# Optimization experiments

Measured on AMD Instinct MI355X. Metric: run time of the kernel, lower is better.

## Reference

```python
import jax, jax.numpy as jnp
import numpy as np

IN_CH = 128
HID = 64
EPS = 1e-5
N_NODES = 20000
E_UND = 80000


def _build_line_graph(edge_index, num_nodes):
    # dedupe to unique undirected edges (src<dst); line-graph nodes = these edges
    src = np.asarray(edge_index[0]); dst = np.asarray(edge_index[1])
    m = src < dst
    u, v = src[m], dst[m]
    key = u.astype(np.int64) * num_nodes + v.astype(np.int64)
    _, first = np.unique(key, return_index=True)
    u, v = u[first], v[first]
    E = u.shape[0]
    # incidence lists grouped by node; all ordered pairs of co-incident edges
    nodes = np.concatenate([u, v])
    eids = np.concatenate([np.arange(E), np.arange(E)])
    order = np.argsort(nodes, kind="stable")
    nodes_s, eids_s = nodes[order], eids[order]
    counts = np.bincount(nodes_s, minlength=num_nodes)
    offsets = np.concatenate([np.zeros(1, np.int64), np.cumsum(counts)])
    grp_start = offsets[nodes_s]
    reps = counts[nodes_s]
    total = int(reps.sum())
    starts = np.cumsum(reps) - reps
    idx = np.arange(total) - np.repeat(starts, reps) + np.repeat(grp_start, reps)
    row = np.repeat(eids_s, reps); col = eids_s[idx]
    keep = row != col
    return np.stack([u, v]), np.stack([row[keep], col[keep]])


def _gcn_conv(x, src, dst, W, b):
    # PyG GCNConv: add self loops, symmetric D^-1/2 (A+I) D^-1/2 normalization
    N = x.shape[0]
    sl = jnp.arange(N)
    s = jnp.concatenate([src, sl]); d = jnp.concatenate([dst, sl])
    deg = jax.ops.segment_sum(jnp.ones(s.shape[0], x.dtype), d, num_segments=N)
    dinv = jax.lax.rsqrt(jnp.maximum(deg, 1.0))
    h = x @ W
    msg = h[s] * (dinv[s] * dinv[d])[:, None]
    return jax.ops.segment_sum(msg, d, num_segments=N) + b


def _edge_scores(line_x, lsrc, ldst, W1, b1, gamma1, beta1, W2, b2):
    h = _gcn_conv(line_x, lsrc, ldst, W1, b1)
    mu = h.mean(0); var = h.var(0)  # BatchNorm1d, training-mode batch stats
    h = jax.nn.relu(gamma1 * (h - mu) * jax.lax.rsqrt(var + EPS) + beta1)
    return jax.nn.sigmoid(_gcn_conv(h, lsrc, ldst, W2, b2))[:, 0]


def _cluster(clean, topk_idx, num_nodes):
    ti = np.asarray(topk_idx)
    sel_src = np.asarray(clean[0])[ti]; sel_dst = np.asarray(clean[1])[ti]
    n2c = np.arange(num_nodes)
    rev = sel_dst[::-1]
    _, fi = np.unique(rev, return_index=True)
    last = sel_dst.shape[0] - 1 - fi
    n2c[sel_dst[last]] = sel_src[last]
    uniq = np.unique(n2c)
    M = int(uniq.shape[0])
    old_to_new = np.full(num_nodes, -1, np.int64)
    old_to_new[uniq] = np.arange(M)
    return old_to_new[n2c], uniq, M


def _make_graph():
    rng = np.random.default_rng(0)
    a = rng.integers(0, N_NODES, E_UND)
    off = rng.integers(1, N_NODES, E_UND)
    b = (a + off) % N_NODES  # no self loops
    u = np.minimum(a, b); v = np.maximum(a, b)
    return np.stack([np.concatenate([u, v]), np.concatenate([v, u])]).astype(np.int64)


def _make_params():
    ks = jax.random.split(jax.random.key(0), 4)
    x = jax.random.normal(ks[0], (N_NODES, IN_CH), jnp.float32)
    W1 = jax.random.normal(ks[1], (IN_CH, HID), jnp.float32) / np.float32(np.sqrt(IN_CH))
    b1 = jnp.zeros((HID,), jnp.float32)
    gamma1 = jnp.ones((HID,), jnp.float32)
    beta1 = jnp.zeros((HID,), jnp.float32)
    W2 = jax.random.normal(ks[2], (HID, 1), jnp.float32) / np.float32(np.sqrt(HID))
    b2 = jnp.zeros((1,), jnp.float32)
    return x, W1, b1, gamma1, beta1, W2, b2


def setup_inputs() -> dict:
    x, W1, b1, gamma1, beta1, W2, b2 = _make_params()
    return {
        "x": x, "W1": W1, "b1": b1, "gamma1": gamma1, "beta1": beta1,
        "W2": W2, "b2": b2,
        "edge_index": jnp.asarray(_make_graph()),
        "batch": jnp.zeros((N_NODES,), jnp.int32),
    }


def reference(x, W1, b1, gamma1, beta1, W2, b2, edge_index, batch):
    N = x.shape[0]
    clean, line_ei = _build_line_graph(edge_index, N)
    csrc = jnp.asarray(clean[0]); cdst = jnp.asarray(clean[1])
    lsrc = jnp.asarray(line_ei[0]); ldst = jnp.asarray(line_ei[1])
    line_x = 0.5 * (x[csrc] + x[cdst])  # line-graph node features
    scores = _edge_scores(line_x, lsrc, ldst, W1, b1, gamma1, beta1, W2, b2)
    E_c = scores.shape[0]
    k = max(1, min(E_c // 2, N // 2))
    _, topk_idx = jax.lax.top_k(scores, k)
    new_indices, uniq, M = _cluster(clean, topk_idx, N)
    ni = jnp.asarray(new_indices)
    # aggregate: per-cluster mean of member node features (code's weights are unused)
    counts = jax.ops.segment_sum(jnp.ones(N, x.dtype), ni, num_segments=M)
    x_pool = jax.ops.segment_sum(x, ni, num_segments=M) / counts[:, None]
    batch_pool = batch[jnp.asarray(uniq)]
    # build_new_edges: relabel, drop self loops, coalesce (sorted unique)
    ei = np.asarray(edge_index)
    ns = new_indices[ei[0]]; nd = new_indices[ei[1]]
    keep = ns != nd
    pk = ns[keep] * M + nd[keep]
    upk = np.unique(pk)
    edge_index_pool = jnp.asarray(np.stack([upk // M, upk % M]))
    return (x_pool, edge_index_pool, batch_pool, scores, ni)
```

## Files before the change

kernel.cpp:

```cpp
#include <hip/hip_runtime.h>
#include <stdint.h>

typedef unsigned long long u64;
typedef unsigned int u32;

#define NND 20000
#define EUA 160000
#define EFE 80000
#define ICH 128
#define HIDC 64
#define SCAN_BS 256
#define NB_N ((NND + 255) / 256)
#define NB_EU ((EUA + 255) / 256)
#define NB_EF ((EFE + 255) / 256)
#define NB_E64 ((EFE * HIDC + 255) / 256)
#define NB_X ((NND * ICH + 255) / 256)
#define NSCAN_B ((NND + SCAN_BS - 1) / SCAN_BS)
#define HIST_BLOCKS 128
#define GEB 64
#define XS_PAD 132
#define NCHAIN 4096
#define OUT_MAX_INIT 3000000
#define BK64 64
#define SEL_BINS 4096


__global__ void kScanA(const int* __restrict__ in, int* __restrict__ out,
                       int* __restrict__ bsums, int n) {
    __shared__ int sh[SCAN_BS];
    int tid = threadIdx.x;
    int i = blockIdx.x * SCAN_BS + tid;
    int v = (i < n) ? in[i] : 0;
    sh[tid] = v;
    __syncthreads();
    for (int o = 1; o < SCAN_BS; o <<= 1) {
        int t = (tid >= o) ? sh[tid - o] : 0;
        __syncthreads();
        sh[tid] += t;
        __syncthreads();
    }
    if (i < n) out[i] = sh[tid] - v;
    if (tid == SCAN_BS - 1) bsums[blockIdx.x] = sh[tid];
}
__global__ void kScanB(int* __restrict__ out, const int* __restrict__ bsums,
                       int n, int nb, int* __restrict__ totalDst) {
    __shared__ int sh[160];
    int tid = threadIdx.x;
    if (tid <= nb) sh[tid] = (tid < nb) ? bsums[tid] : 0;
    __syncthreads();
    if (tid == 0) {
        int acc = 0;
        for (int i = 0; i < nb; i++) { int t = sh[i]; sh[i] = acc; acc += t; }
        sh[nb] = acc;
    }
    __syncthreads();
    int i = blockIdx.x * SCAN_BS + tid;
    if (i < n) out[i] += sh[blockIdx.x];
    if (i == 0) {
        int tot = sh[nb];
        out[n] = tot;
        *totalDst = tot;
    }
}

__global__ void kFilterScatter64(const int* __restrict__ ei, int* __restrict__ cnt,
                                 int* __restrict__ bucketV) {
    int i = blockIdx.x * 256 + threadIdx.x;
    if (i >= EUA) return;
    int s = ei[i], d = ei[EUA + i];
    if (s < d) {
        int p = atomicAdd(&cnt[s], 1);
        bucketV[(s << 6) + p] = d;
    }
}
__global__ void kRankSort64(const int* __restrict__ in, int* __restrict__ out,
                            const int* __restrict__ lenA, int* __restrict__ ucnt) {
    int a = blockIdx.x;
    int len = lenA[a];
    int base = a << 6;
    for (int j = threadIdx.x; j < len; j += 64) {
        int v = in[base + j];
        int r = 0;
        for (int i = 0; i < len; i++) {
            int w = in[base + i];
            r += (w < v) || (w == v && i < j);
        }
        out[base + r] = v;
    }
    __syncthreads();
    int c = 0;
    for (int j = threadIdx.x; j < len; j += 64)
        c += (j == 0) || (out[base + j] != out[base + j - 1]);
#pragma unroll
    for (int o = 32; o > 0; o >>= 1) c += __shfl_down(c, o, 64);
    if (threadIdx.x == 0) ucnt[a] = c;
}
__global__ void kCompactInc(const int* __restrict__ arr, const int* __restrict__ cnt,
                            const int* __restrict__ uoff, int* __restrict__ eU,
                            int* __restrict__ eV, int* __restrict__ icnt) {
    int u = blockIdx.x * 256 + threadIdx.x;
    if (u >= NND) return;
    int s = u << 6, e = s + cnt[u], o = uoff[u];
    int myc = 0;
    for (int i = s; i < e; i++)
        if (i == s || arr[i] != arr[i - 1]) {
            int v = arr[i];
            eU[o] = u; eV[o] = v; o++;
            atomicAdd(&icnt[v], 1);
            myc++;
        }
    if (myc) atomicAdd(&icnt[u], myc);
}

__global__ void kIncScatterDinv64(const int* __restrict__ eU, const int* __restrict__ eV,
                                  const int* __restrict__ scal, int* __restrict__ itmp,
                                  int* __restrict__ ilist, const int* __restrict__ icnt,
                                  float* __restrict__ dinv) {
    int e = blockIdx.x * 256 + threadIdx.x;
    if (e >= scal[0]) return;
    int u = eU[e], v = eV[e];
    ilist[(u << 6) + atomicAdd(&itmp[u], 1)] = e;
    ilist[(v << 6) + atomicAdd(&itmp[v], 1)] = e;
    dinv[e] = rsqrtf((float)(icnt[u] + icnt[v] - 1));
}

__global__ void kGemm(const float* __restrict__ x, const float* __restrict__ W1,
                      const int* __restrict__ eU, const int* __restrict__ eV,
                      const int* __restrict__ scal, float* __restrict__ h) {
    __shared__ float W1s[ICH][HIDC];
    __shared__ float xs[GEB][XS_PAD];
    int t = threadIdx.x;
    int E = scal[0];
    int e0 = blockIdx.x * GEB;
    if (e0 >= E) return;

    {
        const float4* Wv = (const float4*)W1;
        float4* Ws = (float4*)&W1s[0][0];
        for (int i = t; i < ICH * HIDC / 4; i += 256) Ws[i] = Wv[i];
    }
    {
        int eb = t >> 2, q = t & 3;
        int e = e0 + eb;
        if (e < E) {
            int u = eU[e], v = eV[e];
            const float4* xu = (const float4*)(x + (size_t)u * ICH) + q * 8;
            const float4* xv = (const float4*)(x + (size_t)v * ICH) + q * 8;
            float* xd = &xs[eb][q * 32];
#pragma unroll
            for (int i = 0; i < 8; i++) {
                float4 a = xu[i], b = xv[i];
                xd[i * 4 + 0] = 0.5f * (a.x + b.x);
                xd[i * 4 + 1] = 0.5f * (a.y + b.y);
                xd[i * 4 + 2] = 0.5f * (a.z + b.z);
                xd[i * 4 + 3] = 0.5f * (a.w + b.w);
            }
        }
    }
    __syncthreads();

    int cg4 = (t & 15) * 4;
    int es = t >> 4;
    float a00=0,a01=0,a02=0,a03=0, a10=0,a11=0,a12=0,a13=0;
    float a20=0,a21=0,a22=0,a23=0, a30=0,a31=0,a32=0,a33=0;
#pragma unroll 4
    for (int k = 0; k < ICH; k++) {
        float4 wv = *(const float4*)&W1s[k][cg4];
        float x0 = xs[es][k], x1 = xs[es + 16][k];
        float x2 = xs[es + 32][k], x3 = xs[es + 48][k];
        a00 += x0 * wv.x; a01 += x0 * wv.y; a02 += x0 * wv.z; a03 += x0 * wv.w;
        a10 += x1 * wv.x; a11 += x1 * wv.y; a12 += x1 * wv.z; a13 += x1 * wv.w;
        a20 += x2 * wv.x; a21 += x2 * wv.y; a22 += x2 * wv.z; a23 += x2 * wv.w;
        a30 += x3 * wv.x; a31 += x3 * wv.y; a32 += x3 * wv.z; a33 += x3 * wv.w;
    }
    int e;
    e = e0 + es;
    if (e < E) *(float4*)&h[(size_t)e * HIDC + cg4] = make_float4(a00, a01, a02, a03);
    e = e0 + es + 16;
    if (e < E) *(float4*)&h[(size_t)e * HIDC + cg4] = make_float4(a10, a11, a12, a13);
    e = e0 + es + 32;
    if (e < E) *(float4*)&h[(size_t)e * HIDC + cg4] = make_float4(a20, a21, a22, a23);
    e = e0 + es + 48;
    if (e < E) *(float4*)&h[(size_t)e * HIDC + cg4] = make_float4(a30, a31, a32, a33);
}

__global__ void kSGather(const float* __restrict__ h, const float* __restrict__ dinv,
                         const int* __restrict__ icnt, const int* __restrict__ ilist,
                         float* __restrict__ S) {
    int n = blockIdx.x;
    int c = threadIdx.x;
    int base = n << 6, len = icnt[n];
    float acc = 0.f;
    for (int j = 0; j < len; j++) {
        int ed = ilist[base + j];
        acc += h[(size_t)ed * HIDC + c] * dinv[ed];
    }
    S[(size_t)n * HIDC + c] = acc;
}
__global__ void kConv1Red1(const float* __restrict__ h, const float* __restrict__ S,
                           const float* __restrict__ dinv, const int* __restrict__ eU,
                           const int* __restrict__ eV, const float* __restrict__ b1,
                           const int* __restrict__ scal, float* __restrict__ h2,
                           float* __restrict__ partial) {
    int t = threadIdx.x;
    int g = blockIdx.x * 4 + (t >> 6);
    int c = t & 63;
    int E = scal[0];
    float bc = b1[c];
    float acc = 0.f;
    for (int e = g; e < E; e += NCHAIN) {
        float a = dinv[e];
        float v = a * (S[(size_t)eU[e] * HIDC + c] + S[(size_t)eV[e] * HIDC + c]) -
                  a * a * h[(size_t)e * HIDC + c] + bc;
        h2[(size_t)e * HIDC + c] = v;
        acc += v;
    }
    partial[g * HIDC + c] = acc;
}
__global__ void kRed1v(const float* __restrict__ h2, const int* __restrict__ scal,
                       const float* __restrict__ muvar, float* __restrict__ partial) {
    int t = threadIdx.x;
    int g = blockIdx.x * 4 + (t >> 6);
    int c = t & 63;
    int E = scal[0];
    float m = muvar[c];
    float acc = 0.f;
    for (int e = g; e < E; e += NCHAIN) {
        float d = h2[(size_t)e * HIDC + c] - m;
        acc += d * d;
    }
    partial[g * HIDC + c] = acc;
}
__global__ void kRed2(const float* __restrict__ partial, const int* __restrict__ scal,
                      float* __restrict__ muvar, int pass) {
    __shared__ float sh[4][HIDC];
    int t = threadIdx.x;
    int q = t >> 6, c = t & 63;
    float acc = 0.f;
    int g0 = q * (NCHAIN / 4);
    for (int g = g0; g < g0 + NCHAIN / 4; g++) acc += partial[g * HIDC + c];
    sh[q][c] = acc;
    __syncthreads();
    if (q == 0) {
        float s = ((sh[0][c] + sh[1][c]) + sh[2][c]) + sh[3][c];
        muvar[pass * HIDC + c] = s / (float)scal[0];
    }
}
__global__ void kNormZ(const float* __restrict__ h2, const float* __restrict__ muvar,
                       const float* __restrict__ gamma1, const float* __restrict__ beta1,
                       const float* __restrict__ W2, const int* __restrict__ scal,
                       float* __restrict__ z) {
    int idx = blockIdx.x * 256 + threadIdx.x;
    int e = idx >> 6;
    if (e >= scal[0]) return;
    int c = idx & 63;
    float t = gamma1[c] * (h2[idx] - muvar[c]) * rsqrtf(muvar[HIDC + c] + 1e-5f) + beta1[c];
    t = t > 0.f ? t : 0.f;
    float p = t * W2[c];
#pragma unroll
    for (int o = 32; o > 0; o >>= 1) p += __shfl_down(p, o, 64);
    if (c == 0) z[e] = p;
}
__global__ void kS2(const float* __restrict__ z, const float* __restrict__ dinv,
                    const int* __restrict__ icnt, const int* __restrict__ ilist,
                    float* __restrict__ S2) {
    int n = blockIdx.x * 256 + threadIdx.x;
    if (n >= NND) return;
    int base = n << 6, len = icnt[n];
    float acc = 0.f;
    for (int j = 0; j < len; j++) {
        int e = ilist[base + j];
        acc += z[e] * dinv[e];
    }
    S2[n] = acc;
}
__global__ void kScore(const float* __restrict__ z, const float* __restrict__ S2,
                       const float* __restrict__ dinv, const int* __restrict__ eU,
                       const int* __restrict__ eV, const float* __restrict__ b2,
                       const int* __restrict__ scal, float* __restrict__ score,
                       u64* __restrict__ okey, int* __restrict__ krem,
                       u64* __restrict__ pref, u64* __restrict__ minOkey) {
    int e = blockIdx.x * 256 + threadIdx.x;
    if (e < NND) minOkey[e] = ~0ULL;
    int E = scal[0];
    if (e >= E) return;
    if (e == 0) {
        int k = E / 2;
        if (k > NND / 2) k = NND / 2;
        if (k < 1) k = 1;
        *krem = k;
        *pref = 1ULL << 48;
    }
    float a = dinv[e];
    float l = a * (S2[eU[e]] + S2[eV[e]]) - a * a * z[e] + b2[0];
    float s = 1.f / (1.f + expf(-l));
    score[e] = s;
    u32 b = __float_as_uint(s);
    b = (b >> 31) ? ~b : (b | 0x80000000u);
    okey[e] = (((u64)b) << 17) | (u32)(0x1FFFFu - (u32)e);
}

__global__ void kHist(const u64* __restrict__ okey, const int* __restrict__ scal,
                      int* __restrict__ hist, const u64* __restrict__ pref,
                      u64 maskHi, int shift) {
    __shared__ int sh[4][SEL_BINS];
    int t = threadIdx.x;
    for (int j = t; j < 4 * SEL_BINS; j += 256) ((int*)sh)[j] = 0;
    __syncthreads();
    int wv = t >> 6;
    int E = scal[0];
    u64 p = *pref;
    for (int e = blockIdx.x * 256 + t; e < E; e += HIST_BLOCKS * 256) {
        u64 kk = okey[e];
        if ((kk & maskHi) == p)
            atomicAdd(&sh[wv][(int)((kk >> shift) & (SEL_BINS - 1))], 1);
    }
    __syncthreads();
    for (int j = t; j < SEL_BINS; j += 256) {
        int v = sh[0][j] + sh[1][j] + sh[2][j] + sh[3][j];
        if (v) atomicAdd(&hist[j], v);
    }
}
__global__ void kSelPass(int* __restrict__ hist, u64* __restrict__ pref,
                         int* __restrict__ krem, int shift) {
    __shared__ int sh[SEL_BINS];
    __shared__ int aux[256];
    __shared__ int shKr;
    int t = threadIdx.x;
    int g = 0;
#pragma unroll
    for (int j = 0; j < 16; j++) {
        int v = hist[16 * t + j];
        sh[16 * t + j] = v;
        hist[16 * t + j] = 0;
        g += v;
    }
    if (t == 0) shKr = *krem;
    aux[t] = g;
    __syncthreads();
    for (int o = 1; o < 256; o <<= 1) {
        int v = (t + o < 256) ? aux[t + o] : 0;
        __syncthreads();
        aux[t] += v;
        __syncthreads();
    }
    int kr = shKr;
    int suf = aux[t] - g;
    if (suf < kr && kr <= suf + g) {
        int cum = suf, found = 16 * t;
        for (int b = 16 * t + 15; b >= 16 * t; b--) {
            int hc = sh[b];
            if (cum + hc >= kr) { found = b; break; }
            cum += hc;
        }
        *krem = kr - cum;
        *pref |= ((u64)found) << shift;
    }
}

__global__ void kMinKeyInit(const u64* __restrict__ okey, const int* __restrict__ eV,
                            const int* __restrict__ scal, const u64* __restrict__ pref,
                            u64* __restrict__ minOkey, int* __restrict__ n2c) {
    int i = blockIdx.x * 256 + threadIdx.x;
    if (i < NND) n2c[i] = i;
    if (i < scal[0]) {
        u64 k = okey[i];
        if (k >= *pref) atomicMin(&minOkey[eV[i]], k);
    }
}
__global__ void kN2cSet(const u64* __restrict__ okey, const int* __restrict__ eU,
                        const int* __restrict__ eV, const int* __restrict__ scal,
                        const u64* __restrict__ pref, const u64* __restrict__ minOkey,
                        int* __restrict__ n2c) {
    int e = blockIdx.x * 256 + threadIdx.x;
    if (e >= scal[0]) return;
    u64 k = okey[e];
    int v = eV[e];
    if (k >= *pref && k == minOkey[v]) n2c[v] = eU[e];
}
__global__ void kPresent(const int* __restrict__ n2c, int* __restrict__ present) {
    int n = blockIdx.x * 256 + threadIdx.x;
    if (n < NND) present[n2c[n]] = 1;
}

__global__ void kNiXacc(const float* __restrict__ x, const int* __restrict__ n2c,
                        const int* __restrict__ o2n, int* __restrict__ ni,
                        int* __restrict__ ccnt, float* __restrict__ dout) {
    int idx = blockIdx.x * 256 + threadIdx.x;
    if (idx >= NND * ICH) return;
    int n = idx >> 7, c = idx & 127;
    int m = o2n[n2c[n]];
    atomicAdd(&dout[(size_t)m * ICH + c], x[idx]);
    if (c == 0) {
        ni[n] = m;
        atomicAdd(&ccnt[m], 1);
    }
}
__global__ void kXdivCEcount(float* __restrict__ dout, const int* __restrict__ ccnt,
                             const int* __restrict__ scal, const int* __restrict__ ei,
                             const int* __restrict__ ni, int* __restrict__ ecnt2) {
    int idx = blockIdx.x * 256 + threadIdx.x;
    if (idx < scal[2] * ICH) dout[idx] /= (float)ccnt[idx >> 7];
    if (idx < EUA) {
        int a = ni[ei[idx]], b = ni[ei[EUA + idx]];
        if (a != b) atomicAdd(&ecnt2[a], 1);
    }
}

__global__ void kCEscatter(const int* __restrict__ ei, const int* __restrict__ ni,
                           const int* __restrict__ eoff2, int* __restrict__ etmp2,
                           int* __restrict__ bkD) {
    int i = blockIdx.x * 256 + threadIdx.x;
    if (i >= EUA) return;
    int a = ni[ei[i]], b = ni[ei[EUA + i]];
    if (a != b) {
        int p = eoff2[a] + atomicAdd(&etmp2[a], 1);
        bkD[p] = b;
    }
}
__global__ void kRankSort(const int* __restrict__ in, int* __restrict__ out,
                          const int* __restrict__ offA, int* __restrict__ ucnt) {
    int a = blockIdx.x;
    int s = offA[a], e = offA[a + 1], len = e - s;
    for (int j = threadIdx.x; j < len; j += 64) {
        int v = in[s + j];
        int r = 0;
        for (int i = 0; i < len; i++) {
            int w = in[s + i];
            r += (w < v) || (w == v && i < j);
        }
        out[s + r] = v;
    }
    __syncthreads();
    int c = 0;
    for (int j = threadIdx.x; j < len; j += 64)
        c += (j == 0) || (out[s + j] != out[s + j - 1]);
#pragma unroll
    for (int o = 32; o > 0; o >>= 1) c += __shfl_down(c, o, 64);
    if (threadIdx.x == 0) ucnt[a] = c;
}
__global__ void kCEwriteTail(const int* __restrict__ bkD2, const int* __restrict__ eoff2,
                             const int* __restrict__ ueoff, const int* __restrict__ scal,
                             const int* __restrict__ batch, const int* __restrict__ present,
                             const int* __restrict__ o2n, const float* __restrict__ score,
                             const int* __restrict__ ni, float* __restrict__ dout) {
    int i = blockIdx.x * 256 + threadIdx.x;
    int E = scal[0], M = scal[2], Ep = scal[3];
    size_t base = (size_t)M * ICH;
    if (i < NND) {
        int s = eoff2[i], e = eoff2[i + 1];
        float* r0 = dout + base;
        float* r1 = r0 + Ep;
        int o = ueoff[i];
        for (int j = s; j < e; j++)
            if (j == s || bkD2[j] != bkD2[j - 1]) {
                r0[o] = (float)i;
                r1[o] = (float)bkD2[j];
                o++;
            }
    }
    size_t tb = base + 2 * (size_t)Ep;
    if (i < NND && present[i]) dout[tb + o2n[i]] = (float)batch[i];
    if (i < E) dout[tb + M + i] = score[i];
    if (i < NND) dout[tb + M + E + i] = (float)ni[i];
}

extern "C" void kernel_launch(void* const* d_in, const int* in_sizes, int n_in,
                              void* d_out, int out_size, void* d_ws, size_t ws_size,
                              hipStream_t stream) {
    (void)in_sizes; (void)n_in; (void)ws_size;
    const float* x = (const float*)d_in[0];
    const float* W1 = (const float*)d_in[1];
    const float* b1 = (const float*)d_in[2];
    const float* gamma1 = (const float*)d_in[3];
    const float* beta1 = (const float*)d_in[4];
    const float* W2 = (const float*)d_in[5];
    const float* b2 = (const float*)d_in[6];
    const int* ei = (const int*)d_in[7];
    const int* batch = (const int*)d_in[8];
    float* dout = (float*)d_out;

    char* w = (char*)d_ws;
    size_t off = 0;
    auto carve = [&](size_t bytes) -> void* {
        off = (off + 255) & ~(size_t)255;
        void* p = w + off;
        off += bytes;
        return p;
    };
    char* zero0 = w;
    int* cnt = (int*)carve(NND * 4);
    int* itmp = (int*)carve(NND * 4);
    int* icnt = (int*)carve(NND * 4);
    int* present = (int*)carve(NND * 4);
    int* ccnt = (int*)carve(NND * 4);
    int* ecnt2 = (int*)carve(NND * 4);
    int* etmp2 = (int*)carve(NND * 4);
    int* scal = (int*)carve(16 * 4);
    int* hist = (int*)carve(SEL_BINS * 4);
    size_t zeroBytes = off;
    int* ucnt = (int*)carve(NND * 4);
    int* uoff = (int*)carve((NND + 2) * 4);
    int* bsums = (int*)carve((NSCAN_B + 2) * 4);
    int* n2c = (int*)carve(NND * 4);
    int* o2n = (int*)carve((NND + 2) * 4);
    int* niArr = (int*)carve(NND * 4);
    int* eoff2 = (int*)carve((NND + 2) * 4);
    int* uecnt = (int*)carve(NND * 4);
    int* ueoff = (int*)carve((NND + 2) * 4);
    int* bucketV = (int*)carve((size_t)NND * BK64 * 4);
    int* bucketS = (int*)carve((size_t)NND * BK64 * 4);
    int* eU = (int*)carve(EFE * 4);
    int* eV = (int*)carve(EFE * 4);
    int* ilist = (int*)carve((size_t)NND * BK64 * 4);
    int* ilistS = (int*)carve((size_t)NND * BK64 * 4);
    int* bkD = (int*)carve(EUA * 4);
    int* bkD2 = (int*)carve(EUA * 4);
    u64* okey = (u64*)carve(EFE * 8);
    u64* minOkey = (u64*)carve(NND * 8);
    u64* dpref = (u64*)carve(8);
    float* dinv = (float*)carve(EFE * 4);
    float* h = (float*)carve((size_t)EFE * HIDC * 4);
    float* h2 = (float*)carve((size_t)EFE * HIDC * 4);
    float* Snode = (float*)carve((size_t)NND * HIDC * 4);
    float* partial = (float*)carve((size_t)NCHAIN * HIDC * 4);
    float* muvar = (float*)carve(128 * 4);
    float* zArr = (float*)carve(EFE * 4);
    float* S2 = (float*)carve(NND * 4);
    float* score = (float*)carve(EFE * 4);

    auto scan = [&](const int* in, int* outp, int* totalDst) {
        kScanA<<<NSCAN_B, SCAN_BS, 0, stream>>>(in, outp, bsums, NND);
        kScanB<<<NSCAN_B, SCAN_BS, 0, stream>>>(outp, bsums, NND, NSCAN_B, totalDst);
    };

    size_t outInit = (size_t)out_size;
    if (outInit > OUT_MAX_INIT) outInit = OUT_MAX_INIT;
    hipMemsetAsync(zero0, 0, zeroBytes, stream);
    hipMemsetAsync(d_out, 0, outInit * 4, stream);

    kFilterScatter64<<<NB_EU, 256, 0, stream>>>(ei, cnt, bucketV);
    kRankSort64<<<NND, 64, 0, stream>>>(bucketV, bucketS, cnt, ucnt);
    scan(ucnt, uoff, scal + 0);
    kCompactInc<<<NB_N, 256, 0, stream>>>(bucketS, cnt, uoff, eU, eV, icnt);

    kIncScatterDinv64<<<NB_EF, 256, 0, stream>>>(eU, eV, scal, itmp, ilist, icnt, dinv);
    kRankSort64<<<NND, 64, 0, stream>>>(ilist, ilistS, icnt, ucnt);

    kGemm<<<(EFE + GEB - 1) / GEB, 256, 0, stream>>>(x, W1, eU, eV, scal, h);
    kSGather<<<NND, HIDC, 0, stream>>>(h, dinv, icnt, ilistS, Snode);
    kConv1Red1<<<NCHAIN / 4, 256, 0, stream>>>(h, Snode, dinv, eU, eV, b1, scal, h2, partial);
    kRed2<<<1, 256, 0, stream>>>(partial, scal, muvar, 0);
    kRed1v<<<NCHAIN / 4, 256, 0, stream>>>(h2, scal, muvar, partial);
    kRed2<<<1, 256, 0, stream>>>(partial, scal, muvar, 1);
    kNormZ<<<NB_E64, 256, 0, stream>>>(h2, muvar, gamma1, beta1, W2, scal, zArr);

    kS2<<<NB_N, 256, 0, stream>>>(zArr, dinv, icnt, ilistS, S2);
    kScore<<<NB_EF, 256, 0, stream>>>(zArr, S2, dinv, eU, eV, b2, scal, score, okey,
                                      scal + 1, dpref, minOkey);

    for (int p = 0; p < 4; p++) {
        int shift = 36 - 12 * p;
        u64 maskHi = (~0ULL) << (shift + 12);
        kHist<<<HIST_BLOCKS, 256, 0, stream>>>(okey, scal, hist, dpref, maskHi, shift);
        kSelPass<<<1, 256, 0, stream>>>(hist, dpref, scal + 1, shift);
    }

    kMinKeyInit<<<NB_EF, 256, 0, stream>>>(okey, eV, scal, dpref, minOkey, n2c);
    kN2cSet<<<NB_EF, 256, 0, stream>>>(okey, eU, eV, scal, dpref, minOkey, n2c);
    kPresent<<<NB_N, 256, 0, stream>>>(n2c, present);
    scan(present, o2n, scal + 2);
    kNiXacc<<<NB_X, 256, 0, stream>>>(x, n2c, o2n, niArr, ccnt, dout);
    kXdivCEcount<<<NB_X, 256, 0, stream>>>(dout, ccnt, scal, ei, niArr, ecnt2);

    scan(ecnt2, eoff2, scal + 4);
    kCEscatter<<<NB_EU, 256, 0, stream>>>(ei, niArr, eoff2, etmp2, bkD);
    kRankSort<<<NND, 64, 0, stream>>>(bkD, bkD2, eoff2, uecnt);
    scan(uecnt, ueoff, scal + 3);
    kCEwriteTail<<<NB_EF, 256, 0, stream>>>(bkD2, eoff2, ueoff, scal, batch, present,
                                            o2n, score, niArr, dout);
}
```

Measured before the change: 401.4 us.

## Fuse radix-select passes by replaying prefix in each histogram block; merge cluster kernels

Removes the four single-block kSelPass launches by keeping one histogram per pass and having every kHistR block (and the min-key kernel) recompute the selected prefix from all earlier histograms. The three kernels for min-key init, n2c set and present marking become two, with the cluster id decoded straight from the winning key's edge index. This cuts kernel launches and serial single-block steps, but every block now redundantly repeats up to four block-wide scans over 4096-bin histograms.

```diff
diff --git a/kernel.cpp b/kernel.cpp
--- a/kernel.cpp
+++ b/kernel.cpp
@@ -278,19 +278,11 @@
                        const float* __restrict__ dinv, const int* __restrict__ eU,
                        const int* __restrict__ eV, const float* __restrict__ b2,
                        const int* __restrict__ scal, float* __restrict__ score,
-                       u64* __restrict__ okey, int* __restrict__ krem,
-                       u64* __restrict__ pref, u64* __restrict__ minOkey) {
+                       u64* __restrict__ okey, u64* __restrict__ minOkey) {
     int e = blockIdx.x * 256 + threadIdx.x;
     if (e < NND) minOkey[e] = ~0ULL;
     int E = scal[0];
     if (e >= E) return;
-    if (e == 0) {
-        int k = E / 2;
-        if (k > NND / 2) k = NND / 2;
-        if (k < 1) k = 1;
-        *krem = k;
-        *pref = 1ULL << 48;
-    }
     float a = dinv[e];
     float l = a * (S2[eU[e]] + S2[eV[e]]) - a * a * z[e] + b2[0];
     float s = 1.f / (1.f + expf(-l));
@@ -300,87 +292,94 @@
     okey[e] = (((u64)b) << 17) | (u32)(0x1FFFFu - (u32)e);
 }
 
-__global__ void kHist(const u64* __restrict__ okey, const int* __restrict__ scal,
-                      int* __restrict__ hist, const u64* __restrict__ pref,
-                      u64 maskHi, int shift) {
+__device__ __forceinline__ u64 selReplay(const int* __restrict__ histBase, int passes,
+                                         int E, int t, int* aux, int* shTmp) {
+    int kr = E / 2;
+    if (kr > NND / 2) kr = NND / 2;
+    if (kr < 1) kr = 1;
+    u64 pref = 1ULL << 48;
+    for (int q = 0; q < passes; q++) {
+        int shift = 36 - 12 * q;
+        const int* hq = histBase + q * SEL_BINS;
+        int b[16];
+        int g = 0;
+#pragma unroll
+        for (int j = 0; j < 16; j++) { b[j] = hq[16 * t + j]; g += b[j]; }
+        aux[t] = g;
+        __syncthreads();
+        for (int o = 1; o < 256; o <<= 1) {
+            int v = (t + o < 256) ? aux[t + o] : 0;
+            __syncthreads();
+            aux[t] += v;
+            __syncthreads();
+        }
+        int suf = aux[t] - g;
+        if (suf < kr && kr <= suf + g) {
+            int cum = suf, found = 16 * t;
+            for (int j = 15; j >= 0; j--) {
+                int hc = b[j];
+                if (cum + hc >= kr) { found = 16 * t + j; break; }
+                cum += hc;
+            }
+            shTmp[0] = found;
+            shTmp[1] = kr - cum;
+        }
+        __syncthreads();
+        pref |= ((u64)shTmp[0]) << shift;
+        kr = shTmp[1];
+        __syncthreads();
+    }
+    return pref;
+}
+__global__ void kHistR(const u64* __restrict__ okey, const int* __restrict__ scal,
+                       int* __restrict__ histBase, int pass) {
     __shared__ int sh[4][SEL_BINS];
+    __shared__ int aux[256];
+    __shared__ int shTmp[2];
     int t = threadIdx.x;
+    int E = scal[0];
+    u64 p = selReplay(histBase, pass, E, t, aux, shTmp);
     for (int j = t; j < 4 * SEL_BINS; j += 256) ((int*)sh)[j] = 0;
     __syncthreads();
     int wv = t >> 6;
-    int E = scal[0];
-    u64 p = *pref;
+    int shift = 36 - 12 * pass;
+    u64 maskHi = (~0ULL) << (shift + 12);
     for (int e = blockIdx.x * 256 + t; e < E; e += HIST_BLOCKS * 256) {
         u64 kk = okey[e];
         if ((kk & maskHi) == p)
             atomicAdd(&sh[wv][(int)((kk >> shift) & (SEL_BINS - 1))], 1);
     }
     __syncthreads();
+    int* hp = histBase + pass * SEL_BINS;
     for (int j = t; j < SEL_BINS; j += 256) {
         int v = sh[0][j] + sh[1][j] + sh[2][j] + sh[3][j];
-        if (v) atomicAdd(&hist[j], v);
-    }
-}
-__global__ void kSelPass(int* __restrict__ hist, u64* __restrict__ pref,
-                         int* __restrict__ krem, int shift) {
-    __shared__ int sh[SEL_BINS];
+        if (v) atomicAdd(&hp[j], v);
+    }
+}
+
+__global__ void kMinKey(const u64* __restrict__ okey, const int* __restrict__ eV,
+                        const int* __restrict__ scal, const int* __restrict__ histBase,
+                        u64* __restrict__ minOkey) {
     __shared__ int aux[256];
-    __shared__ int shKr;
+    __shared__ int shTmp[2];
     int t = threadIdx.x;
-    int g = 0;
-#pragma unroll
-    for (int j = 0; j < 16; j++) {
-        int v = hist[16 * t + j];
-        sh[16 * t + j] = v;
-        hist[16 * t + j] = 0;
-        g += v;
-    }
-    if (t == 0) shKr = *krem;
-    aux[t] = g;
-    __syncthreads();
-    for (int o = 1; o < 256; o <<= 1) {
-        int v = (t + o < 256) ? aux[t + o] : 0;
-        __syncthreads();
-        aux[t] += v;
-        __syncthreads();
-    }
-    int kr = shKr;
-    int suf = aux[t] - g;
-    if (suf < kr && kr <= suf + g) {
-        int cum = suf, found = 16 * t;
-        for (int b = 16 * t + 15; b >= 16 * t; b--) {
-            int hc = sh[b];
-            if (cum + hc >= kr) { found = b; break; }
-            cum += hc;
-        }
-        *krem = kr - cum;
-        *pref |= ((u64)found) << shift;
-    }
-}
-
-__global__ void kMinKeyInit(const u64* __restrict__ okey, const int* __restrict__ eV,
-                            const int* __restrict__ scal, const u64* __restrict__ pref,
-                            u64* __restrict__ minOkey, int* __restrict__ n2c) {
-    int i = blockIdx.x * 256 + threadIdx.x;
-    if (i < NND) n2c[i] = i;
-    if (i < scal[0]) {
+    int E = scal[0];
+    u64 pref = selReplay(histBase, 4, E, t, aux, shTmp);
+    int i = blockIdx.x * 256 + t;
+    if (i < E) {
         u64 k = okey[i];
-        if (k >= *pref) atomicMin(&minOkey[eV[i]], k);
-    }
-}
-__global__ void kN2cSet(const u64* __restrict__ okey, const int* __restrict__ eU,
-                        const int* __restrict__ eV, const int* __restrict__ scal,
-                        const u64* __restrict__ pref, const u64* __restrict__ minOkey,
-                        int* __restrict__ n2c) {
-    int e = blockIdx.x * 256 + threadIdx.x;
-    if (e >= scal[0]) return;
-    u64 k = okey[e];
-    int v = eV[e];
-    if (k >= *pref && k == minOkey[v]) n2c[v] = eU[e];
-}
-__global__ void kPresent(const int* __restrict__ n2c, int* __restrict__ present) {
-    int n = blockIdx.x * 256 + threadIdx.x;
-    if (n < NND) present[n2c[n]] = 1;
+        if (k >= pref) atomicMin(&minOkey[eV[i]], k);
+    }
+}
+__global__ void kCluster(const u64* __restrict__ minOkey, const int* __restrict__ eU,
+                         int* __restrict__ n2c, int* __restrict__ present) {
+    int v = blockIdx.x * 256 + threadIdx.x;
+    if (v >= NND) return;
+    u64 mk = minOkey[v];
+    int m = v;
+    if (mk != ~0ULL) m = eU[0x1FFFFu - (u32)(mk & 0x1FFFFu)];
+    n2c[v] = m;
+    present[m] = 1;
 }
 
 __global__ void kNiXacc(const float* __restrict__ x, const int* __restrict__ n2c,
@@ -497,7 +496,7 @@
     int* ecnt2 = (int*)carve(NND * 4);
     int* etmp2 = (int*)carve(NND * 4);
     int* scal = (int*)carve(16 * 4);
-    int* hist = (int*)carve(SEL_BINS * 4);
+    int* hist4 = (int*)carve((size_t)4 * SEL_BINS * 4);
     size_t zeroBytes = off;
     int* ucnt = (int*)carve(NND * 4);
     int* uoff = (int*)carve((NND + 2) * 4);
@@ -518,7 +517,6 @@
     int* bkD2 = (int*)carve(EUA * 4);
     u64* okey = (u64*)carve(EFE * 8);
     u64* minOkey = (u64*)carve(NND * 8);
-    u64* dpref = (u64*)carve(8);
     float* dinv = (float*)carve(EFE * 4);
     float* h = (float*)carve((size_t)EFE * HIDC * 4);
     float* h2 = (float*)carve((size_t)EFE * HIDC * 4);
@@ -557,18 +555,13 @@
 
     kS2<<<NB_N, 256, 0, stream>>>(zArr, dinv, icnt, ilistS, S2);
     kScore<<<NB_EF, 256, 0, stream>>>(zArr, S2, dinv, eU, eV, b2, scal, score, okey,
-                                      scal + 1, dpref, minOkey);
-
-    for (int p = 0; p < 4; p++) {
-        int shift = 36 - 12 * p;
-        u64 maskHi = (~0ULL) << (shift + 12);
-        kHist<<<HIST_BLOCKS, 256, 0, stream>>>(okey, scal, hist, dpref, maskHi, shift);
-        kSelPass<<<1, 256, 0, stream>>>(hist, dpref, scal + 1, shift);
-    }
-
-    kMinKeyInit<<<NB_EF, 256, 0, stream>>>(okey, eV, scal, dpref, minOkey, n2c);
-    kN2cSet<<<NB_EF, 256, 0, stream>>>(okey, eU, eV, scal, dpref, minOkey, n2c);
-    kPresent<<<NB_N, 256, 0, stream>>>(n2c, present);
+                                      minOkey);
+
+    for (int p = 0; p < 4; p++)
+        kHistR<<<HIST_BLOCKS, 256, 0, stream>>>(okey, scal, hist4, p);
+
+    kMinKey<<<NB_EF, 256, 0, stream>>>(okey, eV, scal, hist4, minOkey);
+    kCluster<<<NB_N, 256, 0, stream>>>(minOkey, eU, n2c, present);
     scan(present, o2n, scal + 2);
     kNiXacc<<<NB_X, 256, 0, stream>>>(x, n2c, o2n, niArr, ccnt, dout);
     kXdivCEcount<<<NB_X, 256, 0, stream>>>(dout, ccnt, scal, ei, niArr, ecnt2);
```

New measurement: 398.0 us. Within noise of the previous version (-0.9%).
